# Kernel optimization log

Hardware: AMD Instinct MI355X
Metric: run time of the kernel (lower is better)

The kernel has to match this reference:

```python
import jax, jax.numpy as jnp
import numpy as np
import math

K_S = 2  # graph power order
K_T = 2  # temporal localization copies
BN_EPS = 1e-5


def setup_inputs() -> dict:
    key = jax.random.key(0)
    ks = jax.random.split(key, 12)
    B, L, N, H, ND = 8, 12, 1024, 32, 16
    AF = H + ND  # all_feat_dim
    return {
        "history_data": jax.random.normal(ks[0], (B, L, N, 1), jnp.float32),
        "node_embedding_d": jax.random.normal(ks[1], (N, ND), jnp.float32),
        "node_embedding_u": jax.random.normal(ks[2], (N, ND), jnp.float32),
        "adj0": jax.random.uniform(ks[3], (N, N), jnp.float32),
        "adj1": jax.random.uniform(ks[4], (N, N), jnp.float32),
        "W1": jax.random.normal(ks[5], (L, 2 * H), jnp.float32) * 0.1,
        "b1": jnp.zeros((2 * H,), jnp.float32),
        "gamma": jnp.ones((2 * H,), jnp.float32),
        "beta": jnp.zeros((2 * H,), jnp.float32),
        "W2": jax.random.normal(ks[6], (2 * H, H), jnp.float32) * 0.1,
        "b2": jnp.zeros((H,), jnp.float32),
        "WQ": jax.random.normal(ks[7], (AF, H), jnp.float32) * 0.1,
        "WK": jax.random.normal(ks[8], (AF, H), jnp.float32) * 0.1,
    }


def _forward(history_data, node_embedding_d, node_embedding_u, adj0, adj1,
             W1, b1, gamma, beta, W2, b2, WQ, WK):
    B, L, N, _ = history_data.shape
    H = W2.shape[1]

    # --- DistanceFunction ---
    X = jnp.transpose(history_data[..., 0], (0, 2, 1)).reshape(B * N, L)  # [B*N, L]
    h = jax.nn.relu(X @ W1 + b1)                                          # [B*N, 2H]
    mu = jnp.mean(h, axis=0)
    var = jnp.var(h, axis=0)  # biased, matches torch BatchNorm1d train norm
    h = (h - mu) * jax.lax.rsqrt(var + BN_EPS) * gamma + beta
    dy_feat = (h @ W2 + b2).reshape(B, N, H)                              # [B, N, H]

    scale = 1.0 / math.sqrt(H)
    adjs = []
    for emb in (node_embedding_d, node_embedding_u):
        feat = jnp.concatenate(
            [dy_feat, jnp.broadcast_to(emb[None], (B,) + emb.shape)], axis=-1)
        Q = feat @ WQ  # [B, N, H]
        K = feat @ WK
        logits = jnp.einsum("bnh,bmh->bnm", Q, K) * scale
        adjs.append(jax.nn.softmax(logits, axis=-1))

    # --- Mask ---
    adjs = [(adj0 + 1e-7)[None] * adjs[0], (adj1 + 1e-7)[None] * adjs[1]]

    # --- Normalizer: diag_embed+bmm is just a row-wise broadcast scale ---
    def norm(g):
        inv = 1.0 / jnp.sum(g, axis=2)
        inv = jnp.where(jnp.isfinite(inv), inv, 0.0)
        return inv[:, :, None] * g
    adjs = [norm(g) for g in adjs]

    # --- MultiOrder (k=1..K_S), zero diagonal ---
    offdiag = 1.0 - jnp.eye(N, dtype=adjs[0].dtype)
    graphs = []
    for g in adjs:
        k_order = g
        graphs.append(k_order * offdiag)
        for _ in range(2, K_S + 1):
            k_order = jnp.einsum("bnm,bmk->bnk", k_order, g)
            graphs.append(k_order * offdiag)

    # --- st_localization: [B,N,N] -> [B,N,K_T*N] (row repeated K_T times) ---
    local = [jnp.broadcast_to(g[:, :, None, :], (B, N, K_T, N)).reshape(B, N, K_T * N)
             for g in graphs]
    return jnp.stack(local, axis=0)  # [2*K_S, B, N, K_T*N]


def reference(history_data, node_embedding_d, node_embedding_u, adj0, adj1,
              W1, b1, gamma, beta, W2, b2, WQ, WK):
    return _forward(history_data, node_embedding_d, node_embedding_u, adj0, adj1,
                    W1, b1, gamma, beta, W2, b2, WQ, WK)
```

## Files before the change

kernel.cpp:

```cpp
#include <hip/hip_runtime.h>

typedef unsigned short u16;
typedef unsigned int   u32;

typedef __bf16 bf16x8 __attribute__((ext_vector_type(8)));
typedef float  f32x4  __attribute__((ext_vector_type(4)));

__device__ __forceinline__ float bf2f(u16 u) {
  u32 x = ((u32)u) << 16; float f; __builtin_memcpy(&f, &x, 4); return f;
}
__device__ __forceinline__ u16 f2bf(float f) {
  u32 x; __builtin_memcpy(&x, &f, 4);
  x += 0x7fffu + ((x >> 16) & 1u);
  return (u16)(x >> 16);
}
__device__ __forceinline__ void gl2lds16(const void* g, void* l) {
  __builtin_amdgcn_global_load_lds((const __attribute__((address_space(1))) void*)g,
                                   (__attribute__((address_space(3))) void*)l, 16, 0, 0);
}

__global__ __launch_bounds__(256) void k_h(const float* __restrict__ hd, const float* __restrict__ W1,
                                           const float* __restrict__ b1, float* __restrict__ h)
{
  __shared__ float w1s[12 * 64];
  __shared__ float b1s[64];
  int t = threadIdx.x;
  for (int idx = t; idx < 768; idx += 256) w1s[idx] = W1[idx];
  if (t < 64) b1s[t] = b1[t];
  __syncthreads();
  int i = blockIdx.x * 256 + t;
  int b = i >> 10, n = i & 1023;
  float x[12];
#pragma unroll
  for (int l = 0; l < 12; ++l) x[l] = hd[(b * 12 + l) * 1024 + n];
  float acc[64];
#pragma unroll
  for (int j = 0; j < 64; ++j) acc[j] = b1s[j];
#pragma unroll
  for (int l = 0; l < 12; ++l) {
    float xl = x[l];
#pragma unroll
    for (int j = 0; j < 64; ++j) acc[j] += xl * w1s[l * 64 + j];
  }
  float4* hv = (float4*)(h + (size_t)i * 64);
#pragma unroll
  for (int j4 = 0; j4 < 16; ++j4) {
    float4 v;
    v.x = fmaxf(acc[j4 * 4 + 0], 0.f);
    v.y = fmaxf(acc[j4 * 4 + 1], 0.f);
    v.z = fmaxf(acc[j4 * 4 + 2], 0.f);
    v.w = fmaxf(acc[j4 * 4 + 3], 0.f);
    hv[j4] = v;
  }
}

__global__ __launch_bounds__(256) void k_stats(const float* __restrict__ h, float* __restrict__ stats)
{
  int t = threadIdx.x;
  size_t base = (size_t)blockIdx.x * 8192;
  float s = 0.f, sq = 0.f;
  for (int it = 0; it < 32; ++it) {
    float v = h[base + it * 256 + t];
    s += v; sq += v * v;
  }
  __shared__ float ls[256], lq[256];
  ls[t] = s; lq[t] = sq;
  __syncthreads();
  if (t < 64) {
    float S = ls[t] + ls[t + 64] + ls[t + 128] + ls[t + 192];
    float Q = lq[t] + lq[t + 64] + lq[t + 128] + lq[t + 192];
    atomicAdd(&stats[t], S);
    atomicAdd(&stats[64 + t], Q);
  }
}

__global__ void k_finalize(const float* __restrict__ stats, const float* __restrict__ gamma,
                           const float* __restrict__ beta, float* __restrict__ ss)
{
  int t = threadIdx.x;
  float mu = stats[t] * (1.f / 8192.f);
  float var = stats[64 + t] * (1.f / 8192.f) - mu * mu;
  float inv = rsqrtf(var + 1e-5f);
  float sc = gamma[t] * inv;
  ss[t] = sc;
  ss[64 + t] = beta[t] - mu * sc;
}

__global__ __launch_bounds__(256) void k_emb(const float* __restrict__ embd, const float* __restrict__ embu,
                                             const float* __restrict__ WQ, const float* __restrict__ WK,
                                             float* __restrict__ embpart)
{
  int g = blockIdx.x * 256 + threadIdx.x;
  int o = g & 31, n = (g >> 5) & 1023, qk = (g >> 15) & 1, e = g >> 16;
  const float* emb = e ? embu : embd;
  const float* W = qk ? WK : WQ;
  float acc = 0.f;
#pragma unroll
  for (int d = 0; d < 16; ++d) acc += emb[n * 16 + d] * W[(32 + d) * 32 + o];
  embpart[g] = acc;
}

__global__ __launch_bounds__(256) void k_dyqk(const float* __restrict__ h, const float* __restrict__ ss,
                                              const float* __restrict__ W2, const float* __restrict__ b2,
                                              const float* __restrict__ WQ, const float* __restrict__ WK,
                                              const float* __restrict__ embpart,
                                              float* __restrict__ QTf, u16* __restrict__ KTb)
{
  __shared__ float w2s[64 * 32], wqs[32 * 32], wks[32 * 32], b2s[32], scs[64], shs[64];
  int t = threadIdx.x;
  for (int idx = t; idx < 2048; idx += 256) w2s[idx] = W2[idx];
  for (int idx = t; idx < 1024; idx += 256) { wqs[idx] = WQ[idx]; wks[idx] = WK[idx]; }
  if (t < 32) b2s[t] = b2[t];
  if (t < 64) { scs[t] = ss[t]; shs[t] = ss[64 + t]; }
  __syncthreads();
  int i = blockIdx.x * 256 + t;
  int b = i >> 10, n = i & 1023;
  float dy[32];
#pragma unroll
  for (int o = 0; o < 32; ++o) dy[o] = b2s[o];
  for (int j = 0; j < 64; ++j) {
    float hj = h[(size_t)i * 64 + j] * scs[j] + shs[j];
#pragma unroll
    for (int o = 0; o < 32; ++o) dy[o] += hj * w2s[j * 32 + o];
  }
  float tq[32], tk[32];
#pragma unroll
  for (int o = 0; o < 32; ++o) { tq[o] = 0.f; tk[o] = 0.f; }
  for (int j = 0; j < 32; ++j) {
    float d = dy[j];
#pragma unroll
    for (int o = 0; o < 32; ++o) { tq[o] += d * wqs[j * 32 + o]; tk[o] += d * wks[j * 32 + o]; }
  }
#pragma unroll
  for (int e = 0; e < 2; ++e) {
    const float* epQ = embpart + ((size_t)(e * 2 + 0) * 1024 + n) * 32;
    const float* epK = embpart + ((size_t)(e * 2 + 1) * 1024 + n) * 32;
    size_t qb = ((size_t)(e * 8 + b) * 32) * 1024 + n;
#pragma unroll
    for (int o = 0; o < 32; ++o) {
      QTf[qb + (size_t)o * 1024] = tq[o] + epQ[o];
      KTb[qb + (size_t)o * 1024] = f2bf(tk[o] + epK[o]);
    }
  }
}

__global__ __launch_bounds__(256) void k_attn(const float* __restrict__ QTf, const u16* __restrict__ KTb,
                                              const float* __restrict__ adj0, const float* __restrict__ adj1,
                                              u16* __restrict__ G, float* __restrict__ out)
{
  int blk = (blockIdx.x & 7) * 64 + (blockIdx.x >> 3);
  int rg = blk & 31, b = (blk >> 5) & 7, e = blk >> 8;
  int t = threadIdx.x;
  int eb = e * 8 + b;
  int wv = t >> 6, lane = t & 63;
  const float* adj = e ? adj1 : adj0;
  const u16* Kp = KTb + ((size_t)eb << 15);
  const float* Qp = QTf + ((size_t)eb << 15);
  u16* Gp = G + ((size_t)eb << 20);
  float* o1 = out + (((size_t)(2 * e) * 8 + b) << 21);
  const float sc = 0.17677669529663687f;
#pragma unroll
  for (int grp = 0; grp < 2; ++grp) {
    int r0 = rg * 32 + wv * 8 + grp * 4;
    float accA[4][8], accB[4][8];
#pragma unroll
    for (int r = 0; r < 4; ++r)
#pragma unroll
      for (int k = 0; k < 8; ++k) { accA[r][k] = 0.f; accB[r][k] = 0.f; }
    for (int hh = 0; hh < 32; ++hh) {
      float4 qv = *(const float4*)(Qp + hh * 1024 + r0);
      uint4 ka = *(const uint4*)(Kp + hh * 1024 + lane * 8);
      uint4 kb = *(const uint4*)(Kp + hh * 1024 + 512 + lane * 8);
      float kf[8] = {bf2f((u16)ka.x), bf2f((u16)(ka.x >> 16)), bf2f((u16)ka.y), bf2f((u16)(ka.y >> 16)),
                     bf2f((u16)ka.z), bf2f((u16)(ka.z >> 16)), bf2f((u16)ka.w), bf2f((u16)(ka.w >> 16))};
      float kg[8] = {bf2f((u16)kb.x), bf2f((u16)(kb.x >> 16)), bf2f((u16)kb.y), bf2f((u16)(kb.y >> 16)),
                     bf2f((u16)kb.z), bf2f((u16)(kb.z >> 16)), bf2f((u16)kb.w), bf2f((u16)(kb.w >> 16))};
#pragma unroll
      for (int k = 0; k < 8; ++k) {
        accA[0][k] += qv.x * kf[k]; accA[1][k] += qv.y * kf[k];
        accA[2][k] += qv.z * kf[k]; accA[3][k] += qv.w * kf[k];
        accB[0][k] += qv.x * kg[k]; accB[1][k] += qv.y * kg[k];
        accB[2][k] += qv.z * kg[k]; accB[3][k] += qv.w * kg[k];
      }
    }
#pragma unroll
    for (int r = 0; r < 4; ++r) {
      int gr = r0 + r;
      const float* arow = adj + ((size_t)gr << 10);
      int mA = lane * 8, mB = 512 + lane * 8;
      float4 a0 = *(const float4*)(arow + mA);
      float4 a1 = *(const float4*)(arow + mA + 4);
      float4 c0 = *(const float4*)(arow + mB);
      float4 c1 = *(const float4*)(arow + mB + 4);
      float af[8] = {a0.x, a0.y, a0.z, a0.w, a1.x, a1.y, a1.z, a1.w};
      float bfv[8] = {c0.x, c0.y, c0.z, c0.w, c1.x, c1.y, c1.z, c1.w};
      float ta[8], tb[8];
      float p = 0.f;
#pragma unroll
      for (int k = 0; k < 8; ++k) { ta[k] = (af[k] + 1e-7f) * __expf(accA[r][k] * sc); p += ta[k]; }
#pragma unroll
      for (int k = 0; k < 8; ++k) { tb[k] = (bfv[k] + 1e-7f) * __expf(accB[r][k] * sc); p += tb[k]; }
#pragma unroll
      for (int off = 32; off > 0; off >>= 1) p += __shfl_xor(p, off);
      float inv = 1.f / p;
      if (!__builtin_isfinite(inv)) inv = 0.f;
      float ga[8], gb[8];
#pragma unroll
      for (int k = 0; k < 8; ++k) { ga[k] = ta[k] * inv; gb[k] = tb[k] * inv; }
      uint4 pa, pb;
      pa.x = f2bf(ga[0]) | ((u32)f2bf(ga[1]) << 16);  pa.y = f2bf(ga[2]) | ((u32)f2bf(ga[3]) << 16);
      pa.z = f2bf(ga[4]) | ((u32)f2bf(ga[5]) << 16);  pa.w = f2bf(ga[6]) | ((u32)f2bf(ga[7]) << 16);
      pb.x = f2bf(gb[0]) | ((u32)f2bf(gb[1]) << 16);  pb.y = f2bf(gb[2]) | ((u32)f2bf(gb[3]) << 16);
      pb.z = f2bf(gb[4]) | ((u32)f2bf(gb[5]) << 16);  pb.w = f2bf(gb[6]) | ((u32)f2bf(gb[7]) << 16);
      *(uint4*)(Gp + ((size_t)gr << 10) + mA) = pa;
      *(uint4*)(Gp + ((size_t)gr << 10) + mB) = pb;
#pragma unroll
      for (int k = 0; k < 8; ++k) {
        if (mA + k == gr) ga[k] = 0.f;
        if (mB + k == gr) gb[k] = 0.f;
      }
      size_t ob = (size_t)gr << 11;
      float4 fa0 = {ga[0], ga[1], ga[2], ga[3]}, fa1 = {ga[4], ga[5], ga[6], ga[7]};
      float4 fb0 = {gb[0], gb[1], gb[2], gb[3]}, fb1 = {gb[4], gb[5], gb[6], gb[7]};
      *(float4*)(o1 + ob + mA) = fa0;         *(float4*)(o1 + ob + mA + 4) = fa1;
      *(float4*)(o1 + ob + mB) = fb0;         *(float4*)(o1 + ob + mB + 4) = fb1;
      *(float4*)(o1 + ob + 1024 + mA) = fa0;  *(float4*)(o1 + ob + 1024 + mA + 4) = fa1;
      *(float4*)(o1 + ob + 1024 + mB) = fb0;  *(float4*)(o1 + ob + 1024 + mB + 4) = fb1;
    }
  }
}

__global__ __launch_bounds__(256) void k_tr(const u16* __restrict__ G, u16* __restrict__ Gt)
{
  __shared__ u16 tile[64 * 66];
  int blk = (blockIdx.x & 7) * 512 + (blockIdx.x >> 3);
  int mat = blk >> 8, tl = blk & 255, ti = tl >> 4, tj = tl & 15;
  size_t mo = (size_t)mat << 20;
  int t = threadIdx.x;
#pragma unroll
  for (int half = 0; half < 2; ++half) {
    int idx = t + half * 256;
    int row = idx >> 3, q = idx & 7;
    uint4 v = *(const uint4*)(G + mo + (size_t)(ti * 64 + row) * 1024 + tj * 64 + q * 8);
    u16* d = &tile[row * 66 + q * 8];
    d[0] = (u16)v.x; d[1] = (u16)(v.x >> 16);
    d[2] = (u16)v.y; d[3] = (u16)(v.y >> 16);
    d[4] = (u16)v.z; d[5] = (u16)(v.z >> 16);
    d[6] = (u16)v.w; d[7] = (u16)(v.w >> 16);
  }
  __syncthreads();
#pragma unroll
  for (int half = 0; half < 2; ++half) {
    int idx = t + half * 256;
    int row = idx >> 3, q = idx & 7;
    u16 s0 = tile[(q * 8 + 0) * 66 + row], s1 = tile[(q * 8 + 1) * 66 + row];
    u16 s2 = tile[(q * 8 + 2) * 66 + row], s3 = tile[(q * 8 + 3) * 66 + row];
    u16 s4 = tile[(q * 8 + 4) * 66 + row], s5 = tile[(q * 8 + 5) * 66 + row];
    u16 s6 = tile[(q * 8 + 6) * 66 + row], s7 = tile[(q * 8 + 7) * 66 + row];
    uint4 v;
    v.x = s0 | ((u32)s1 << 16); v.y = s2 | ((u32)s3 << 16);
    v.z = s4 | ((u32)s5 << 16); v.w = s6 | ((u32)s7 << 16);
    *(uint4*)(Gt + mo + (size_t)(tj * 64 + row) * 1024 + ti * 64 + q * 8) = v;
  }
}

__global__ __launch_bounds__(256) void k_gemm(const u16* __restrict__ G, const u16* __restrict__ Gt,
                                              float* __restrict__ out)
{
  __shared__ __align__(16) u16 As[2][128 * 32];
  __shared__ __align__(16) u16 Bs[2][128 * 32];
  int bid = (blockIdx.x & 7) * 128 + (blockIdx.x >> 3);
  int mat = bid >> 6, tile = bid & 63, ti = tile >> 3, tj = tile & 7;
  size_t mo = (size_t)mat << 20;
  const u16* A = G + mo;
  const u16* Bm = Gt + mo;
  int t = threadIdx.x;
  int w = t >> 6, lane = t & 63;
  int quad = lane >> 4, l16 = lane & 15;
  int wr = (w & 1) * 64, wc = (w >> 1) * 64;
  f32x4 acc[4][4];
#pragma unroll
  for (int i = 0; i < 4; ++i)
#pragma unroll
    for (int j = 0; j < 4; ++j) acc[i][j] = f32x4{0.f, 0.f, 0.f, 0.f};

#define STAGE(buf, kk)                                                                  \
  {                                                                                     \
    _Pragma("unroll")                                                                   \
    for (int it = 0; it < 2; ++it) {                                                    \
      int sbase = (it * 4 + w) * 64;                                                    \
      int r = (sbase + lane) >> 2, c = (sbase + lane) & 3;                              \
      gl2lds16(A + (size_t)(ti * 128 + r) * 1024 + (kk) + c * 8,                        \
               (u16*)As[buf] + (size_t)sbase * 8);                                      \
      gl2lds16(Bm + (size_t)(tj * 128 + r) * 1024 + (kk) + c * 8,                       \
               (u16*)Bs[buf] + (size_t)sbase * 8);                                      \
    }                                                                                   \
  }

  STAGE(0, 0);
  __syncthreads();
  int cur = 0;
  for (int k0 = 0; k0 < 1024; k0 += 32) {
    if (k0 + 32 < 1024) STAGE(cur ^ 1, k0 + 32);
    bf16x8 af[4], bfr[4];
#pragma unroll
    for (int mt = 0; mt < 4; ++mt)
      af[mt] = *(const bf16x8*)&As[cur][(wr + mt * 16 + l16) * 32 + quad * 8];
#pragma unroll
    for (int nt = 0; nt < 4; ++nt)
      bfr[nt] = *(const bf16x8*)&Bs[cur][(wc + nt * 16 + l16) * 32 + quad * 8];
#pragma unroll
    for (int mt = 0; mt < 4; ++mt)
#pragma unroll
      for (int nt = 0; nt < 4; ++nt)
        acc[mt][nt] = __builtin_amdgcn_mfma_f32_16x16x32_bf16(af[mt], bfr[nt], acc[mt][nt], 0, 0, 0);
    __syncthreads();
    cur ^= 1;
  }
#undef STAGE
  int e = mat >> 3, bb = mat & 7;
  float* o2 = out + (((size_t)(2 * e + 1) * 8 + bb) << 21);
#pragma unroll
  for (int mt = 0; mt < 4; ++mt)
#pragma unroll
    for (int r = 0; r < 4; ++r) {
      int gr = ti * 128 + wr + mt * 16 + quad * 4 + r;
      size_t rb = (size_t)gr << 11;
#pragma unroll
      for (int nt = 0; nt < 4; ++nt) {
        int gc = tj * 128 + wc + nt * 16 + l16;
        float v = (gr == gc) ? 0.f : acc[mt][nt][r];
        o2[rb + gc] = v;
        o2[rb + 1024 + gc] = v;
      }
    }
}

extern "C" void kernel_launch(void* const* d_in, const int* in_sizes, int n_in,
                              void* d_out, int out_size, void* d_ws, size_t ws_size,
                              hipStream_t stream) {
  const float* hd    = (const float*)d_in[0];
  const float* embd  = (const float*)d_in[1];
  const float* embu  = (const float*)d_in[2];
  const float* adj0  = (const float*)d_in[3];
  const float* adj1  = (const float*)d_in[4];
  const float* W1    = (const float*)d_in[5];
  const float* b1    = (const float*)d_in[6];
  const float* gamma = (const float*)d_in[7];
  const float* beta  = (const float*)d_in[8];
  const float* W2    = (const float*)d_in[9];
  const float* b2    = (const float*)d_in[10];
  const float* WQ    = (const float*)d_in[11];
  const float* WK    = (const float*)d_in[12];
  char* ws = (char*)d_ws;
  float* stats   = (float*)(ws + 0);
  float* ss      = (float*)(ws + 1024);
  float* embpart = (float*)(ws + 4096);
  float* h       = (float*)(ws + 528384);
  float* QTf     = (float*)(ws + 2625536);
  u16* KTb       = (u16*)(ws + 4722688);
  u16* G         = (u16*)(ws + 5771264);
  u16* Gt        = (u16*)(ws + 39325696);
  float* out     = (float*)d_out;

  hipMemsetAsync(stats, 0, 512, stream);
  k_h<<<32, 256, 0, stream>>>(hd, W1, b1, h);
  k_stats<<<64, 256, 0, stream>>>(h, stats);
  k_finalize<<<1, 64, 0, stream>>>(stats, gamma, beta, ss);
  k_emb<<<512, 256, 0, stream>>>(embd, embu, WQ, WK, embpart);
  k_dyqk<<<32, 256, 0, stream>>>(h, ss, W2, b2, WQ, WK, embpart, QTf, KTb);
  k_attn<<<512, 256, 0, stream>>>(QTf, KTb, adj0, adj1, G, out);
  k_tr<<<4096, 256, 0, stream>>>(G, Gt);
  k_gemm<<<1024, 256, 0, stream>>>(G, Gt, out);
}
```

Baseline: 416.8 us.

## Drop explicit transpose kernel; load B via ds_read_b64_tr_b16 transposed LDS reads

Removes the separate k_tr transpose pass that wrote Gt, and has the GEMM stage B tiles directly from G in row-major k layout with a permuted staging order. The B fragments are then read with the gfx950 ds_read_b64_tr_b16 transposing LDS instruction. This removes a full read-plus-write pass over 16 bf16 1024x1024 matrices and one kernel launch. In exchange it relies on inline asm with an explicit lgkmcnt wait and a sched barrier, which may limit overlap inside the GEMM loop.

```diff
diff --git a/kernel.cpp b/kernel.cpp
--- a/kernel.cpp
+++ b/kernel.cpp
@@ -5,6 +5,7 @@
 
 typedef __bf16 bf16x8 __attribute__((ext_vector_type(8)));
 typedef float  f32x4  __attribute__((ext_vector_type(4)));
+typedef u32    u32x2  __attribute__((ext_vector_type(2)));
 
 __device__ __forceinline__ float bf2f(u16 u) {
   u32 x = ((u32)u) << 16; float f; __builtin_memcpy(&f, &x, 4); return f;
@@ -230,69 +231,44 @@
   }
 }
 
-__global__ __launch_bounds__(256) void k_tr(const u16* __restrict__ G, u16* __restrict__ Gt)
-{
-  __shared__ u16 tile[64 * 66];
-  int blk = (blockIdx.x & 7) * 512 + (blockIdx.x >> 3);
-  int mat = blk >> 8, tl = blk & 255, ti = tl >> 4, tj = tl & 15;
-  size_t mo = (size_t)mat << 20;
-  int t = threadIdx.x;
-#pragma unroll
-  for (int half = 0; half < 2; ++half) {
-    int idx = t + half * 256;
-    int row = idx >> 3, q = idx & 7;
-    uint4 v = *(const uint4*)(G + mo + (size_t)(ti * 64 + row) * 1024 + tj * 64 + q * 8);
-    u16* d = &tile[row * 66 + q * 8];
-    d[0] = (u16)v.x; d[1] = (u16)(v.x >> 16);
-    d[2] = (u16)v.y; d[3] = (u16)(v.y >> 16);
-    d[4] = (u16)v.z; d[5] = (u16)(v.z >> 16);
-    d[6] = (u16)v.w; d[7] = (u16)(v.w >> 16);
-  }
-  __syncthreads();
-#pragma unroll
-  for (int half = 0; half < 2; ++half) {
-    int idx = t + half * 256;
-    int row = idx >> 3, q = idx & 7;
-    u16 s0 = tile[(q * 8 + 0) * 66 + row], s1 = tile[(q * 8 + 1) * 66 + row];
-    u16 s2 = tile[(q * 8 + 2) * 66 + row], s3 = tile[(q * 8 + 3) * 66 + row];
-    u16 s4 = tile[(q * 8 + 4) * 66 + row], s5 = tile[(q * 8 + 5) * 66 + row];
-    u16 s6 = tile[(q * 8 + 6) * 66 + row], s7 = tile[(q * 8 + 7) * 66 + row];
-    uint4 v;
-    v.x = s0 | ((u32)s1 << 16); v.y = s2 | ((u32)s3 << 16);
-    v.z = s4 | ((u32)s5 << 16); v.w = s6 | ((u32)s7 << 16);
-    *(uint4*)(Gt + mo + (size_t)(tj * 64 + row) * 1024 + ti * 64 + q * 8) = v;
-  }
-}
-
-__global__ __launch_bounds__(256) void k_gemm(const u16* __restrict__ G, const u16* __restrict__ Gt,
-                                              float* __restrict__ out)
+__global__ __launch_bounds__(256) void k_gemm(const u16* __restrict__ G, float* __restrict__ out)
 {
   __shared__ __align__(16) u16 As[2][128 * 32];
-  __shared__ __align__(16) u16 Bs[2][128 * 32];
+  __shared__ __align__(16) u16 Bs[2][4096];
   int bid = (blockIdx.x & 7) * 128 + (blockIdx.x >> 3);
   int mat = bid >> 6, tile = bid & 63, ti = tile >> 3, tj = tile & 7;
   size_t mo = (size_t)mat << 20;
   const u16* A = G + mo;
-  const u16* Bm = Gt + mo;
   int t = threadIdx.x;
   int w = t >> 6, lane = t & 63;
   int quad = lane >> 4, l16 = lane & 15;
   int wr = (w & 1) * 64, wc = (w >> 1) * 64;
+  int s_n0 = wc >> 4;
   f32x4 acc[4][4];
 #pragma unroll
   for (int i = 0; i < 4; ++i)
 #pragma unroll
     for (int j = 0; j < 4; ++j) acc[i][j] = f32x4{0.f, 0.f, 0.f, 0.f};
+
+  const u16* bsrc[2];
+#pragma unroll
+  for (int it = 0; it < 2; ++it) {
+    int c = (it * 4 + w) * 64 + lane;
+    int u = (c >> 3) & 7, j = (c >> 1) & 3;
+    int klocal = ((u & 3) << 3) + ((u >> 2) << 2) + j;
+    bsrc[it] = A + (size_t)klocal * 1024 + tj * 128 + ((c >> 6) & 7) * 16 + (c & 1) * 8;
+  }
 
 #define STAGE(buf, kk)                                                                  \
   {                                                                                     \
     _Pragma("unroll")                                                                   \
     for (int it = 0; it < 2; ++it) {                                                    \
       int sbase = (it * 4 + w) * 64;                                                    \
-      int r = (sbase + lane) >> 2, c = (sbase + lane) & 3;                              \
-      gl2lds16(A + (size_t)(ti * 128 + r) * 1024 + (kk) + c * 8,                        \
+      int sA = sbase + lane;                                                            \
+      int r = sA >> 2, cc = sA & 3;                                                     \
+      gl2lds16(A + (size_t)(ti * 128 + r) * 1024 + (kk) + cc * 8,                       \
                (u16*)As[buf] + (size_t)sbase * 8);                                      \
-      gl2lds16(Bm + (size_t)(tj * 128 + r) * 1024 + (kk) + c * 8,                       \
+      gl2lds16(bsrc[it] + (size_t)(kk) * 1024,                                          \
                (u16*)Bs[buf] + (size_t)sbase * 8);                                      \
     }                                                                                   \
   }
@@ -302,13 +278,27 @@
   int cur = 0;
   for (int k0 = 0; k0 < 1024; k0 += 32) {
     if (k0 + 32 < 1024) STAGE(cur ^ 1, k0 + 32);
-    bf16x8 af[4], bfr[4];
+    bf16x8 af[4];
 #pragma unroll
     for (int mt = 0; mt < 4; ++mt)
       af[mt] = *(const bf16x8*)&As[cur][(wr + mt * 16 + l16) * 32 + quad * 8];
-#pragma unroll
-    for (int nt = 0; nt < 4; ++nt)
-      bfr[nt] = *(const bf16x8*)&Bs[cur][(wc + nt * 16 + l16) * 32 + quad * 8];
+    u32 bb = (u32)(size_t)(const __attribute__((address_space(3))) u16*)&Bs[cur][0];
+    u32 laddr = bb + (u32)lane * 8;
+    u32x2 r1[4], r2[4];
+#pragma unroll
+    for (int nt = 0; nt < 4; ++nt) {
+      u32 a = laddr + (u32)(s_n0 + nt) * 1024;
+      asm volatile("ds_read_b64_tr_b16 %0, %1" : "=v"(r1[nt]) : "v"(a));
+      asm volatile("ds_read_b64_tr_b16 %0, %1 offset:512" : "=v"(r2[nt]) : "v"(a));
+    }
+    asm volatile("s_waitcnt lgkmcnt(0)" ::: "memory");
+    __builtin_amdgcn_sched_barrier(0);
+    bf16x8 bfr[4];
+#pragma unroll
+    for (int nt = 0; nt < 4; ++nt) {
+      u32 tmp[4] = {r1[nt].x, r1[nt].y, r2[nt].x, r2[nt].y};
+      __builtin_memcpy(&bfr[nt], tmp, 16);
+    }
 #pragma unroll
     for (int mt = 0; mt < 4; ++mt)
 #pragma unroll
@@ -318,8 +308,8 @@
     cur ^= 1;
   }
 #undef STAGE
-  int e = mat >> 3, bb = mat & 7;
-  float* o2 = out + (((size_t)(2 * e + 1) * 8 + bb) << 21);
+  int e = mat >> 3, bb2 = mat & 7;
+  float* o2 = out + (((size_t)(2 * e + 1) * 8 + bb2) << 21);
 #pragma unroll
   for (int mt = 0; mt < 4; ++mt)
 #pragma unroll
@@ -360,7 +350,6 @@
   float* QTf     = (float*)(ws + 2625536);
   u16* KTb       = (u16*)(ws + 4722688);
   u16* G         = (u16*)(ws + 5771264);
-  u16* Gt        = (u16*)(ws + 39325696);
   float* out     = (float*)d_out;
 
   hipMemsetAsync(stats, 0, 512, stream);
@@ -370,6 +359,5 @@
   k_emb<<<512, 256, 0, stream>>>(embd, embu, WQ, WK, embpart);
   k_dyqk<<<32, 256, 0, stream>>>(h, ss, W2, b2, WQ, WK, embpart, QTf, KTb);
   k_attn<<<512, 256, 0, stream>>>(QTf, KTb, adj0, adj1, G, out);
-  k_tr<<<4096, 256, 0, stream>>>(G, Gt);
-  k_gemm<<<1024, 256, 0, stream>>>(G, Gt, out);
-}
+  k_gemm<<<1024, 256, 0, stream>>>(G, out);
+}
```

Result: faster. 403.9 us (-3.1%).
